# Kernel tuning notes

Hardware: AMD Instinct MI355X
Metric: run time of the kernel (lower is better)

## Reference

```python
import jax, jax.numpy as jnp
import numpy as np

NUM_SEGMENTS = 1024  # number of distinct group ids in ix (fill_max)
DIM = 384


def setup_inputs() -> dict:
    key = jax.random.key(0)
    ks = jax.random.split(key, 8)
    H = 65536
    x = jax.random.normal(ks[0], (1, H, DIM), dtype=jnp.float32)
    ix = jax.random.randint(ks[1], (1, H), 0, NUM_SEGMENTS, dtype=jnp.int64)
    s = 0.05  # keep g(x) in a numerically tame range before exp
    f_w = jax.random.normal(ks[2], (DIM, DIM), dtype=jnp.float32) * s
    f_b = jax.random.normal(ks[3], (DIM,), dtype=jnp.float32) * s
    g_w = jax.random.normal(ks[4], (DIM, DIM), dtype=jnp.float32) * s
    g_b = jax.random.normal(ks[5], (DIM,), dtype=jnp.float32) * s
    h_w = jax.random.normal(ks[6], (DIM, DIM), dtype=jnp.float32) * s
    h_b = jax.random.normal(ks[7], (DIM,), dtype=jnp.float32) * s
    return {"x": x, "ix": ix, "f_w": f_w, "f_b": f_b, "g_w": g_w,
            "g_b": g_b, "h_w": h_w, "h_b": h_b}


def reference(x, ix, f_w, f_b, g_w, g_b, h_w, h_b):
    # x: [1, H, C]; ix: [1, H] group ids. Original builds an [H,H] equality
    # mask; the math is exactly a per-group softmax(g(x))-weighted sum of f(x)
    # broadcast back to every member of the group, so we use segment_sum.
    ix0 = ix[0]                                   # [H]
    fx = x[0] @ f_w.T + f_b                       # [H, C]
    gx = jnp.clip(x[0] @ g_w.T + g_b, -50.0, 50.0)
    w = jnp.exp(gx)                               # [H, C]
    denom = jax.ops.segment_sum(w, ix0, num_segments=NUM_SEGMENTS)  # [S, C]
    denom = jnp.maximum(denom, 1e-9)
    wi = w / denom[ix0]                           # normalized weights, [H, C]
    num = jax.ops.segment_sum(fx * wi, ix0, num_segments=NUM_SEGMENTS)  # [S, C]
    y = num[ix0][None]                            # [1, H, C]
    return y @ h_w.T + h_b
```

## Files before the change

### kernel.cpp

```cpp
#include <hip/hip_runtime.h>

#define DIM 384
#define NSEG 1024
#define CHUNK 32
#define LDA 392
#define MAXLS 8
#define NHB 16

typedef __attribute__((ext_vector_type(8))) short bf16x8;
typedef __attribute__((ext_vector_type(4))) float f32x4;

static __device__ __forceinline__ short f2bf(float f) {
    union { float f; unsigned u; } v{f};
    unsigned r = (v.u + 0x7FFFu + ((v.u >> 16) & 1u)) >> 16;
    return (short)r;
}

#define PACKB ((2 * 24 * 12 * 64) / 1024)

__global__ __launch_bounds__(1024) void prep_kernel(
    const int* __restrict__ ix, int* __restrict__ hist_part,
    const float* __restrict__ fw, const float* __restrict__ gw,
    short* __restrict__ pb, int H) {
    __shared__ int lh[NSEG];
    int b = blockIdx.x;
    int t = threadIdx.x;
    if (b < PACKB) {
        int idx = b * 1024 + t;
        int lane = idx & 63;
        int ks   = (idx >> 6) % 12;
        int T    = ((idx >> 6) / 12) % 24;
        int mat  = idx / (64 * 12 * 24);
        const float* src = mat ? gw : fw;
        int ch = T * 16 + (lane & 15);
        int k0 = ks * 32 + (lane >> 4) * 8;
        short* dst = pb + (size_t)idx * 8;
#pragma unroll
        for (int e = 0; e < 8; e++) dst[e] = f2bf(src[(size_t)ch * DIM + k0 + e]);
    } else {
        int hb = b - PACKB;
        lh[t] = 0;
        __syncthreads();
        int rpb = (H + NHB - 1) / NHB;
        int lo = hb * rpb;
        int hi = lo + rpb; if (hi > H) hi = H;
        for (int i = lo + t; i < hi; i += 1024)
            atomicAdd(&lh[ix[i]], 1);
        __syncthreads();
        hist_part[hb * NSEG + t] = lh[t];
    }
}

__global__ __launch_bounds__(1024) void scan_kernel(
    const int* __restrict__ hist_part, int* __restrict__ seg_start,
    int* __restrict__ cursor) {
    __shared__ int wsum[16];
    int t = threadIdx.x;
    int v = 0;
#pragma unroll
    for (int b = 0; b < NHB; b++) v += hist_part[b * NSEG + t];
    int lane = t & 63, wv = t >> 6;
    int s = v;
#pragma unroll
    for (int off = 1; off < 64; off <<= 1) {
        int u = __shfl_up(s, off, 64);
        if (lane >= off) s += u;
    }
    if (lane == 63) wsum[wv] = s;
    __syncthreads();
    if (wv == 0) {
        int ws = (lane < 16) ? wsum[lane] : 0;
#pragma unroll
        for (int off = 1; off < 16; off <<= 1) {
            int u = __shfl_up(ws, off, 64);
            if (lane >= off) ws += u;
        }
        if (lane < 16) wsum[lane] = ws;
    }
    __syncthreads();
    int incl = s + (wv ? wsum[wv - 1] : 0);
    seg_start[t] = incl - v;
    cursor[t]    = incl - v;
    if (t == NSEG - 1) seg_start[NSEG] = incl;
}

__global__ __launch_bounds__(1024) void scatter_kernel(
    const int* __restrict__ ix, int* __restrict__ cursor,
    int* __restrict__ order, int H) {
    __shared__ int lbase[NSEG];
    __shared__ int lcur[NSEG];
    int t = threadIdx.x;
    int rpb = (H + gridDim.x - 1) / gridDim.x;
    int lo = blockIdx.x * rpb;
    int hi = lo + rpb; if (hi > H) hi = H;
    lbase[t] = 0;
    __syncthreads();
    for (int i = lo + t; i < hi; i += 1024)
        atomicAdd(&lbase[ix[i]], 1);
    __syncthreads();
    int c = lbase[t];
    int base = (c > 0) ? atomicAdd(&cursor[t], c) : 0;
    __syncthreads();
    lbase[t] = base;
    lcur[t] = 0;
    __syncthreads();
    for (int i = lo + t; i < hi; i += 1024) {
        int sg = ix[i];
        int p = lbase[sg] + atomicAdd(&lcur[sg], 1);
        order[p] = i;
    }
}

__global__ __launch_bounds__(512, 4) void seg_gemm_chunk(
    const float* __restrict__ x, const short* __restrict__ pb,
    const float* __restrict__ f_b, const float* __restrict__ g_b,
    const int* __restrict__ order, const int* __restrict__ ix,
    float* __restrict__ den_acc, float* __restrict__ num_acc) {
    const int chunk0 = blockIdx.x * CHUNK;
    const int tid  = threadIdx.x;
    const int lane = tid & 63;
    const int wave = tid >> 6;
    const int n    = lane & 15;
    const int q    = lane >> 4;
    const int cb   = wave * 48;

    __shared__ short As[CHUNK * LDA];
    __shared__ int   segrow[CHUNK];

    {
        int r  = tid >> 4;
        int c6 = tid & 15;
        int gr = order[chunk0 + r];
        if (c6 == 0) segrow[r] = ix[gr];
        const f32x4* xr = (const f32x4*)(x + (size_t)gr * DIM);
        short* dst = &As[r * LDA];
#pragma unroll
        for (int i = 0; i < 6; i++) {
            f32x4 v = __builtin_nontemporal_load(xr + c6 + 16 * i);
            short4 s = { f2bf(v[0]), f2bf(v[1]), f2bf(v[2]), f2bf(v[3]) };
            *(short4*)&dst[(c6 + 16 * i) * 4] = s;
        }
    }
    __syncthreads();

    float fbv[3], gbv[3];
#pragma unroll
    for (int t = 0; t < 3; t++) {
        fbv[t] = f_b[cb + t * 16 + n];
        gbv[t] = g_b[cb + t * 16 + n];
    }

    f32x4 accf[2][3], accg[2][3];
#pragma unroll
    for (int rt = 0; rt < 2; rt++)
#pragma unroll
        for (int t = 0; t < 3; t++) {
            accf[rt][t] = (f32x4){0.f, 0.f, 0.f, 0.f};
            accg[rt][t] = (f32x4){0.f, 0.f, 0.f, 0.f};
        }

#pragma unroll
    for (int ks = 0; ks < 12; ks++) {
        bf16x8 a[2];
#pragma unroll
        for (int rt = 0; rt < 2; rt++)
            a[rt] = *(const bf16x8*)&As[(rt * 16 + n) * LDA + ks * 32 + q * 8];
#pragma unroll
        for (int t = 0; t < 3; t++) {
            int Tg = wave * 3 + t;
            bf16x8 bfr = *(const bf16x8*)(pb + ((size_t)((0 * 24 + Tg) * 12 + ks)) * 512 + lane * 8);
            bf16x8 bgr = *(const bf16x8*)(pb + ((size_t)((1 * 24 + Tg) * 12 + ks)) * 512 + lane * 8);
#pragma unroll
            for (int rt = 0; rt < 2; rt++) {
                accf[rt][t] = __builtin_amdgcn_mfma_f32_16x16x32_bf16(a[rt], bfr, accf[rt][t], 0, 0, 0);
                accg[rt][t] = __builtin_amdgcn_mfma_f32_16x16x32_bf16(a[rt], bgr, accg[rt][t], 0, 0, 0);
            }
        }
    }

    const int s0 = segrow[0];
    __syncthreads();
    float* accs = (float*)As;
    for (int i = tid; i < MAXLS * DIM * 2; i += 512) accs[i] = 0.f;
    __syncthreads();

#pragma unroll
    for (int t = 0; t < 3; t++) {
        int ch = cb + t * 16 + n;
        float rw = 0.f, rf = 0.f;
        int cur = -1;
#pragma unroll
        for (int rt = 0; rt < 2; rt++) {
#pragma unroll
            for (int r = 0; r < 4; r++) {
                int m  = rt * 16 + q * 4 + r;
                int ls = segrow[m] - s0;
                if (ls != cur) {
                    if (cur >= 0) {
                        if (cur < MAXLS) {
                            atomicAdd(&accs[(cur * DIM + ch) * 2 + 0], rw);
                            atomicAdd(&accs[(cur * DIM + ch) * 2 + 1], rf);
                        } else {
                            atomicAdd(&den_acc[(size_t)(s0 + cur) * DIM + ch], rw);
                            atomicAdd(&num_acc[(size_t)(s0 + cur) * DIM + ch], rf);
                        }
                    }
                    cur = ls; rw = 0.f; rf = 0.f;
                }
                float gx = accg[rt][t][r] + gbv[t];
                gx = fmaxf(-50.f, fminf(50.f, gx));
                float w = __expf(gx);
                rw += w;
                rf += (accf[rt][t][r] + fbv[t]) * w;
            }
        }
        if (cur < MAXLS) {
            atomicAdd(&accs[(cur * DIM + ch) * 2 + 0], rw);
            atomicAdd(&accs[(cur * DIM + ch) * 2 + 1], rf);
        } else {
            atomicAdd(&den_acc[(size_t)(s0 + cur) * DIM + ch], rw);
            atomicAdd(&num_acc[(size_t)(s0 + cur) * DIM + ch], rf);
        }
    }
    __syncthreads();

    int nls = segrow[CHUNK - 1] - s0 + 1;
    if (nls > MAXLS) nls = MAXLS;
    for (int i = tid; i < nls * DIM; i += 512) {
        int ls = i / DIM, ch = i - ls * DIM;
        float dw = accs[(ls * DIM + ch) * 2 + 0];
        float dn = accs[(ls * DIM + ch) * 2 + 1];
        if (dw != 0.f || dn != 0.f) {
            atomicAdd(&den_acc[(size_t)(s0 + ls) * DIM + ch], dw);
            atomicAdd(&num_acc[(size_t)(s0 + ls) * DIM + ch], dn);
        }
    }
}

__global__ __launch_bounds__(256) void hgemm_kernel(
    const float* __restrict__ num, const float* __restrict__ den,
    const float* __restrict__ h_w, const float* __restrict__ h_b,
    float* __restrict__ z) {
    const int m0 = blockIdx.x * 64;
    const int c0 = blockIdx.y * 64;
    const int tid = threadIdx.x;
    const int ty = tid >> 4, tx = tid & 15;
    __shared__ float As[16][64];
    __shared__ float Bs[16][64];
    float acc[4][4];
#pragma unroll
    for (int i = 0; i < 4; i++)
#pragma unroll
        for (int j = 0; j < 4; j++) acc[i][j] = 0.f;

    for (int k0 = 0; k0 < DIM; k0 += 16) {
        __syncthreads();
        {
            int m  = tid >> 2;
            int kq = (tid & 3) << 2;
            size_t idx = (size_t)(m0 + m) * DIM + k0 + kq;
            float4 v = *(const float4*)(num + idx);
            float4 d = *(const float4*)(den + idx);
            v.x /= fmaxf(d.x, 1e-9f); v.y /= fmaxf(d.y, 1e-9f);
            v.z /= fmaxf(d.z, 1e-9f); v.w /= fmaxf(d.w, 1e-9f);
            As[kq + 0][m] = v.x; As[kq + 1][m] = v.y;
            As[kq + 2][m] = v.z; As[kq + 3][m] = v.w;
            float4 w = *(const float4*)(h_w + (size_t)(c0 + m) * DIM + k0 + kq);
            Bs[kq + 0][m] = w.x; Bs[kq + 1][m] = w.y;
            Bs[kq + 2][m] = w.z; Bs[kq + 3][m] = w.w;
        }
        __syncthreads();
#pragma unroll
        for (int kk = 0; kk < 16; kk++) {
            float4 a4 = *(const float4*)&As[kk][ty * 4];
            float4 b4 = *(const float4*)&Bs[kk][tx * 4];
            float a[4] = { a4.x, a4.y, a4.z, a4.w };
            float b[4] = { b4.x, b4.y, b4.z, b4.w };
#pragma unroll
            for (int i = 0; i < 4; i++)
#pragma unroll
                for (int j = 0; j < 4; j++) acc[i][j] += a[i] * b[j];
        }
    }
#pragma unroll
    for (int i = 0; i < 4; i++)
#pragma unroll
        for (int j = 0; j < 4; j++)
            z[(size_t)(m0 + ty * 4 + i) * DIM + c0 + tx * 4 + j] = acc[i][j] + h_b[c0 + tx * 4 + j];
}

__global__ void gather_kernel(const int* __restrict__ ix, const f32x4* __restrict__ z,
                              f32x4* __restrict__ out, int H) {
    int t = blockIdx.x * blockDim.x + threadIdx.x;
    int total = H * (DIM / 4);
    if (t < total) {
        int i = t / (DIM / 4);
        int qq = t - i * (DIM / 4);
        f32x4 v = z[(size_t)ix[i] * (DIM / 4) + qq];
        __builtin_nontemporal_store(v, out + (size_t)i * (DIM / 4) + qq);
    }
}

extern "C" void kernel_launch(void* const* d_in, const int* in_sizes, int n_in,
                              void* d_out, int out_size, void* d_ws, size_t ws_size,
                              hipStream_t stream) {
    const float* x   = (const float*)d_in[0];
    const int*   ix  = (const int*)d_in[1];
    const float* f_w = (const float*)d_in[2];
    const float* f_b = (const float*)d_in[3];
    const float* g_w = (const float*)d_in[4];
    const float* g_b = (const float*)d_in[5];
    const float* h_w = (const float*)d_in[6];
    const float* h_b = (const float*)d_in[7];
    float* out = (float*)d_out;
    const int H = in_sizes[0] / DIM;

    char* w = (char*)d_ws;
    int* hist_part = (int*)w;   w += NHB * NSEG * 4;
    int* seg_start = (int*)w;   w += 8192;
    int* cursor    = (int*)w;   w += 4096;
    int* order     = (int*)w;   w += (size_t)H * 4;
    float* den_acc = (float*)w; w += (size_t)NSEG * DIM * 4;
    float* num_acc = (float*)w; w += (size_t)NSEG * DIM * 4;
    float* z       = (float*)w; w += (size_t)NSEG * DIM * 4;
    short* pb      = (short*)w;

    (void)hipMemsetAsync(den_acc, 0, (size_t)2 * NSEG * DIM * 4, stream);
    prep_kernel<<<PACKB + NHB, 1024, 0, stream>>>(ix, hist_part, f_w, g_w, pb, H);
    scan_kernel<<<1, NSEG, 0, stream>>>(hist_part, seg_start, cursor);
    scatter_kernel<<<NHB, 1024, 0, stream>>>(ix, cursor, order, H);
    seg_gemm_chunk<<<H / CHUNK, 512, 0, stream>>>(x, pb, f_b, g_b, order, ix,
                                                  den_acc, num_acc);
    hgemm_kernel<<<dim3(NSEG / 64, DIM / 64), 256, 0, stream>>>(num_acc, den_acc,
                                                                h_w, h_b, z);
    gather_kernel<<<(H * (DIM / 4) + 255) / 256, 256, 0, stream>>>(
        ix, (const f32x4*)z, (f32x4*)out, H);
}
```

Before: 312.6 us.

## Assign one block per segment with double-buffered row staging, removing atomics

The segment GEMM kernel changes from fixed 32-row chunks, which spread segment partials through shared and global atomics, to one block per segment. Each block loops over its segment's sorted rows in 32-row chunks, prefetching the next chunk's x rows into a second LDS buffer while the MFMAs run. It reduces in registers and writes den/num directly, so the memset and atomics go away. The histogram block count also rises to 64 for more parallelism in prep and scatter. The risk is load imbalance: per-segment lengths vary, and only 1024 blocks are launched.

After: 658.9 us. 2.11x slower.

```diff
diff --git a/kernel.cpp b/kernel.cpp
--- a/kernel.cpp
+++ b/kernel.cpp
@@ -2,10 +2,8 @@
 
 #define DIM 384
 #define NSEG 1024
-#define CHUNK 32
 #define LDA 392
-#define MAXLS 8
-#define NHB 16
+#define NHB 64
 
 typedef __attribute__((ext_vector_type(8))) short bf16x8;
 typedef __attribute__((ext_vector_type(4))) float f32x4;
@@ -57,7 +55,7 @@
     __shared__ int wsum[16];
     int t = threadIdx.x;
     int v = 0;
-#pragma unroll
+#pragma unroll 8
     for (int b = 0; b < NHB; b++) v += hist_part[b * NSEG + t];
     int lane = t & 63, wv = t >> 6;
     int s = v;
@@ -111,12 +109,17 @@
     }
 }
 
-__global__ __launch_bounds__(512, 4) void seg_gemm_chunk(
+__global__ __launch_bounds__(512, 4) void seg_gemm_seg(
     const float* __restrict__ x, const short* __restrict__ pb,
     const float* __restrict__ f_b, const float* __restrict__ g_b,
-    const int* __restrict__ order, const int* __restrict__ ix,
-    float* __restrict__ den_acc, float* __restrict__ num_acc) {
-    const int chunk0 = blockIdx.x * CHUNK;
+    const int* __restrict__ order, const int* __restrict__ seg_start,
+    float* __restrict__ den, float* __restrict__ num) {
+    const int s = blockIdx.x;
+    const int b = seg_start[s];
+    const int e = seg_start[s + 1];
+    const int len = e - b;
+    const int nch = (len + 31) >> 5;
+
     const int tid  = threadIdx.x;
     const int lane = tid & 63;
     const int wave = tid >> 6;
@@ -124,24 +127,10 @@
     const int q    = lane >> 4;
     const int cb   = wave * 48;
 
-    __shared__ short As[CHUNK * LDA];
-    __shared__ int   segrow[CHUNK];
-
-    {
-        int r  = tid >> 4;
-        int c6 = tid & 15;
-        int gr = order[chunk0 + r];
-        if (c6 == 0) segrow[r] = ix[gr];
-        const f32x4* xr = (const f32x4*)(x + (size_t)gr * DIM);
-        short* dst = &As[r * LDA];
-#pragma unroll
-        for (int i = 0; i < 6; i++) {
-            f32x4 v = __builtin_nontemporal_load(xr + c6 + 16 * i);
-            short4 s = { f2bf(v[0]), f2bf(v[1]), f2bf(v[2]), f2bf(v[3]) };
-            *(short4*)&dst[(c6 + 16 * i) * 4] = s;
-        }
-    }
-    __syncthreads();
+    __shared__ short As[2][32 * LDA];
+
+    const int r  = tid >> 4;
+    const int c6 = tid & 15;
 
     float fbv[3], gbv[3];
 #pragma unroll
@@ -150,89 +139,110 @@
         gbv[t] = g_b[cb + t * 16 + n];
     }
 
-    f32x4 accf[2][3], accg[2][3];
-#pragma unroll
-    for (int rt = 0; rt < 2; rt++)
+    float sw[3] = {0.f, 0.f, 0.f}, sf[3] = {0.f, 0.f, 0.f};
+
+    if (nch > 0) {
+        f32x4 sv[6];
+#pragma unroll
+        for (int i = 0; i < 6; i++) sv[i] = (f32x4){0.f, 0.f, 0.f, 0.f};
+        int r0 = b + r;
+        if (r0 < e) {
+            int gr = order[r0];
+            const f32x4* xr = (const f32x4*)(x + (size_t)gr * DIM);
+#pragma unroll
+            for (int i = 0; i < 6; i++) sv[i] = __builtin_nontemporal_load(xr + c6 + 16 * i);
+        }
+        short* dst = &As[0][r * LDA];
+#pragma unroll
+        for (int i = 0; i < 6; i++) {
+            short4 sx = { f2bf(sv[i][0]), f2bf(sv[i][1]), f2bf(sv[i][2]), f2bf(sv[i][3]) };
+            *(short4*)&dst[(c6 + 16 * i) * 4] = sx;
+        }
+        __syncthreads();
+    }
+
+    for (int c = 0; c < nch; c++) {
+        const int cur = c & 1;
+        const bool hn = (c + 1) < nch;
+
+        f32x4 sv[6];
+#pragma unroll
+        for (int i = 0; i < 6; i++) sv[i] = (f32x4){0.f, 0.f, 0.f, 0.f};
+        if (hn) {
+            int r2 = b + (c + 1) * 32 + r;
+            if (r2 < e) {
+                int gr = order[r2];
+                const f32x4* xr = (const f32x4*)(x + (size_t)gr * DIM);
+#pragma unroll
+                for (int i = 0; i < 6; i++) sv[i] = __builtin_nontemporal_load(xr + c6 + 16 * i);
+            }
+        }
+
+        f32x4 accf[2][3], accg[2][3];
+#pragma unroll
+        for (int rt = 0; rt < 2; rt++)
+#pragma unroll
+            for (int t = 0; t < 3; t++) {
+                accf[rt][t] = (f32x4){0.f, 0.f, 0.f, 0.f};
+                accg[rt][t] = (f32x4){0.f, 0.f, 0.f, 0.f};
+            }
+
+#pragma unroll
+        for (int ks = 0; ks < 12; ks++) {
+            bf16x8 a[2];
+#pragma unroll
+            for (int rt = 0; rt < 2; rt++)
+                a[rt] = *(const bf16x8*)&As[cur][(rt * 16 + n) * LDA + ks * 32 + q * 8];
+#pragma unroll
+            for (int t = 0; t < 3; t++) {
+                int Tg = wave * 3 + t;
+                bf16x8 bfr = *(const bf16x8*)(pb + ((size_t)((0 * 24 + Tg) * 12 + ks)) * 512 + lane * 8);
+                bf16x8 bgr = *(const bf16x8*)(pb + ((size_t)((1 * 24 + Tg) * 12 + ks)) * 512 + lane * 8);
+#pragma unroll
+                for (int rt = 0; rt < 2; rt++) {
+                    accf[rt][t] = __builtin_amdgcn_mfma_f32_16x16x32_bf16(a[rt], bfr, accf[rt][t], 0, 0, 0);
+                    accg[rt][t] = __builtin_amdgcn_mfma_f32_16x16x32_bf16(a[rt], bgr, accg[rt][t], 0, 0, 0);
+                }
+            }
+        }
+
+        const int rowbase = c * 32;
 #pragma unroll
         for (int t = 0; t < 3; t++) {
-            accf[rt][t] = (f32x4){0.f, 0.f, 0.f, 0.f};
-            accg[rt][t] = (f32x4){0.f, 0.f, 0.f, 0.f};
-        }
-
-#pragma unroll
-    for (int ks = 0; ks < 12; ks++) {
-        bf16x8 a[2];
-#pragma unroll
-        for (int rt = 0; rt < 2; rt++)
-            a[rt] = *(const bf16x8*)&As[(rt * 16 + n) * LDA + ks * 32 + q * 8];
-#pragma unroll
-        for (int t = 0; t < 3; t++) {
-            int Tg = wave * 3 + t;
-            bf16x8 bfr = *(const bf16x8*)(pb + ((size_t)((0 * 24 + Tg) * 12 + ks)) * 512 + lane * 8);
-            bf16x8 bgr = *(const bf16x8*)(pb + ((size_t)((1 * 24 + Tg) * 12 + ks)) * 512 + lane * 8);
 #pragma unroll
             for (int rt = 0; rt < 2; rt++) {
-                accf[rt][t] = __builtin_amdgcn_mfma_f32_16x16x32_bf16(a[rt], bfr, accf[rt][t], 0, 0, 0);
-                accg[rt][t] = __builtin_amdgcn_mfma_f32_16x16x32_bf16(a[rt], bgr, accg[rt][t], 0, 0, 0);
-            }
-        }
-    }
-
-    const int s0 = segrow[0];
-    __syncthreads();
-    float* accs = (float*)As;
-    for (int i = tid; i < MAXLS * DIM * 2; i += 512) accs[i] = 0.f;
-    __syncthreads();
+#pragma unroll
+                for (int rr = 0; rr < 4; rr++) {
+                    int m = rt * 16 + q * 4 + rr;
+                    float gx = accg[rt][t][rr] + gbv[t];
+                    gx = fmaxf(-50.f, fminf(50.f, gx));
+                    float w = __expf(gx);
+                    float wv = (rowbase + m < len) ? w : 0.f;
+                    sw[t] += wv;
+                    sf[t] += (accf[rt][t][rr] + fbv[t]) * wv;
+                }
+            }
+        }
+
+        if (hn) {
+            short* dst = &As[cur ^ 1][r * LDA];
+#pragma unroll
+            for (int i = 0; i < 6; i++) {
+                short4 sx = { f2bf(sv[i][0]), f2bf(sv[i][1]), f2bf(sv[i][2]), f2bf(sv[i][3]) };
+                *(short4*)&dst[(c6 + 16 * i) * 4] = sx;
+            }
+        }
+        __syncthreads();
+    }
 
 #pragma unroll
     for (int t = 0; t < 3; t++) {
-        int ch = cb + t * 16 + n;
-        float rw = 0.f, rf = 0.f;
-        int cur = -1;
-#pragma unroll
-        for (int rt = 0; rt < 2; rt++) {
-#pragma unroll
-            for (int r = 0; r < 4; r++) {
-                int m  = rt * 16 + q * 4 + r;
-                int ls = segrow[m] - s0;
-                if (ls != cur) {
-                    if (cur >= 0) {
-                        if (cur < MAXLS) {
-                            atomicAdd(&accs[(cur * DIM + ch) * 2 + 0], rw);
-                            atomicAdd(&accs[(cur * DIM + ch) * 2 + 1], rf);
-                        } else {
-                            atomicAdd(&den_acc[(size_t)(s0 + cur) * DIM + ch], rw);
-                            atomicAdd(&num_acc[(size_t)(s0 + cur) * DIM + ch], rf);
-                        }
-                    }
-                    cur = ls; rw = 0.f; rf = 0.f;
-                }
-                float gx = accg[rt][t][r] + gbv[t];
-                gx = fmaxf(-50.f, fminf(50.f, gx));
-                float w = __expf(gx);
-                rw += w;
-                rf += (accf[rt][t][r] + fbv[t]) * w;
-            }
-        }
-        if (cur < MAXLS) {
-            atomicAdd(&accs[(cur * DIM + ch) * 2 + 0], rw);
-            atomicAdd(&accs[(cur * DIM + ch) * 2 + 1], rf);
-        } else {
-            atomicAdd(&den_acc[(size_t)(s0 + cur) * DIM + ch], rw);
-            atomicAdd(&num_acc[(size_t)(s0 + cur) * DIM + ch], rf);
-        }
-    }
-    __syncthreads();
-
-    int nls = segrow[CHUNK - 1] - s0 + 1;
-    if (nls > MAXLS) nls = MAXLS;
-    for (int i = tid; i < nls * DIM; i += 512) {
-        int ls = i / DIM, ch = i - ls * DIM;
-        float dw = accs[(ls * DIM + ch) * 2 + 0];
-        float dn = accs[(ls * DIM + ch) * 2 + 1];
-        if (dw != 0.f || dn != 0.f) {
-            atomicAdd(&den_acc[(size_t)(s0 + ls) * DIM + ch], dw);
-            atomicAdd(&num_acc[(size_t)(s0 + ls) * DIM + ch], dn);
+        float d  = sw[t], nm = sf[t];
+        d  += __shfl_xor(d, 16, 64);  d  += __shfl_xor(d, 32, 64);
+        nm += __shfl_xor(nm, 16, 64); nm += __shfl_xor(nm, 32, 64);
+        if (q == 0) {
+            den[(size_t)s * DIM + cb + t * 16 + n] = d;
+            num[(size_t)s * DIM + cb + t * 16 + n] = nm;
         }
     }
 }
@@ -325,12 +335,11 @@
     float* z       = (float*)w; w += (size_t)NSEG * DIM * 4;
     short* pb      = (short*)w;
 
-    (void)hipMemsetAsync(den_acc, 0, (size_t)2 * NSEG * DIM * 4, stream);
     prep_kernel<<<PACKB + NHB, 1024, 0, stream>>>(ix, hist_part, f_w, g_w, pb, H);
     scan_kernel<<<1, NSEG, 0, stream>>>(hist_part, seg_start, cursor);
     scatter_kernel<<<NHB, 1024, 0, stream>>>(ix, cursor, order, H);
-    seg_gemm_chunk<<<H / CHUNK, 512, 0, stream>>>(x, pb, f_b, g_b, order, ix,
-                                                  den_acc, num_acc);
+    seg_gemm_seg<<<NSEG, 512, 0, stream>>>(x, pb, f_b, g_b, order, seg_start,
+                                           den_acc, num_acc);
     hgemm_kernel<<<dim3(NSEG / 64, DIM / 64), 256, 0, stream>>>(num_acc, den_acc,
                                                                 h_w, h_b, z);
     gather_kernel<<<(H * (DIM / 4) + 255) / 256, 256, 0, stream>>>(
```
